# Optimization experiments

Measured on AMD Instinct MI355X. Metric: run time of the kernel, lower is better.

The kernel has to match this reference:

```python
import jax, jax.numpy as jnp
import numpy as np

B, T, H = 32, 4096, 512


def setup_inputs() -> dict:
    key = jax.random.key(0)
    k1, k2, k3, k4, k5 = jax.random.split(key, 5)
    stdv = 1.0 / np.sqrt(2 * H)
    stdv_v = 1.0 / np.sqrt(H)
    return {
        "hidden": jax.random.normal(k1, (B, H), dtype=jnp.float32),
        "encoder_outputs": jax.random.normal(k2, (T, B, H), dtype=jnp.float32),
        "W_attn": jax.random.uniform(k3, (H, 2 * H), minval=-stdv, maxval=stdv, dtype=jnp.float32),
        "b_attn": jax.random.uniform(k4, (H,), minval=-stdv, maxval=stdv, dtype=jnp.float32),
        "v": jax.random.uniform(k5, (H,), minval=-stdv_v, maxval=stdv_v, dtype=jnp.float32),
    }


def reference(hidden, encoder_outputs, W_attn, b_attn, v):
    # hidden: [B, H]; encoder_outputs: [T, B, H]
    T_ = encoder_outputs.shape[0]
    h = jnp.broadcast_to(hidden[None, :, :], (T_,) + hidden.shape).transpose(1, 0, 2)  # [B,T,H]
    enc = encoder_outputs.transpose(1, 0, 2)  # [B,T,H]
    cat = jnp.concatenate([h, enc], axis=2)  # [B,T,2H]
    # Linear(2H -> H) then legacy F.softmax with implicit dim=0 for 3D input (batch axis)
    energy = jax.nn.softmax(jnp.einsum('btk,hk->bth', cat, W_attn) + b_attn, axis=0)  # [B,T,H]
    # bmm(v[B,1,H], energy^T[B,H,T]) -> [B,1,T] -> squeeze -> [B,T]
    scores = jnp.einsum('h,bth->bt', v, energy)
    return jax.nn.relu(scores)[:, None, :]  # [B,1,T]
```

## Files before the change

### kernel.cpp

```cpp
#include <hip/hip_runtime.h>
#include <hip/hip_bf16.h>

#define B_ 32
#define T_ 4096
#define H_ 512
#define TILE_T 4
#define M_TILE 128
#define BK 64
#define KSTEPS 8
#define NTHREADS 512

typedef __attribute__((ext_vector_type(8))) short short8;
typedef __attribute__((ext_vector_type(8))) __bf16 bf16x8;
typedef __attribute__((ext_vector_type(4))) float f32x4;

__device__ __forceinline__ short f2bf(float f) {
    unsigned u = __builtin_bit_cast(unsigned, f);
    u = (u + 0x7fffu + ((u >> 16) & 1u)) >> 16;
    return (short)u;
}

__global__ void prep_w2(const float* __restrict__ W, short* __restrict__ w2p) {
    int idx = blockIdx.x * 256 + threadIdx.x;
    int kp = idx & 63;
    int h  = (idx >> 6) & 511;
    int s  = idx >> 15;
    int k  = kp ^ ((h & 7) << 3);
    w2p[idx] = f2bf(W[h * (2 * H_) + H_ + s * BK + k]);
}

__global__ void prep_hid(const float* __restrict__ hidden,
                         const float* __restrict__ W,
                         const float* __restrict__ bias,
                         float* __restrict__ hidproj) {
    __shared__ float hrow[H_];
    int b = blockIdx.y;
    int h = blockIdx.x * 128 + threadIdx.x;
    for (int i = threadIdx.x; i < H_; i += 128) hrow[i] = hidden[b * H_ + i];
    __syncthreads();
    const float* wr = W + (size_t)h * (2 * H_);
    float acc = bias[h];
#pragma unroll 4
    for (int k = 0; k < H_; k += 4) {
        acc += hrow[k]     * wr[k];
        acc += hrow[k + 1] * wr[k + 1];
        acc += hrow[k + 2] * wr[k + 2];
        acc += hrow[k + 3] * wr[k + 3];
    }
    hidproj[b * H_ + h] = acc;
}

__global__ __launch_bounds__(NTHREADS, 2)
void attn_main(const float* __restrict__ enc,
               const float* __restrict__ hidproj,
               const short* __restrict__ w2p,
               const float* __restrict__ vvec,
               float* __restrict__ out)
{
    __shared__ __align__(16) short lds_a[M_TILE * BK];
    __shared__ __align__(16) short lds_w[H_ * BK];

    const int tid  = threadIdx.x;
    const int lane = tid & 63;
    const int wid  = tid >> 6;
    const int t0   = blockIdx.x * TILE_T;
    const int n0   = wid * 64;
    const int lo   = lane & 15;
    const int hi4  = lane >> 4;

    f32x4 acc[8][4];
#pragma unroll
    for (int i = 0; i < 8; ++i)
#pragma unroll
        for (int j = 0; j < 4; ++j) acc[i][j] = f32x4{0.f, 0.f, 0.f, 0.f};

    const int s0row = tid >> 3;
    const int s0ks  = tid & 7;
    const float* encbase = enc + (size_t)(t0 * B_) * H_;

    for (int kk = 0; kk < KSTEPS; ++kk) {
        const short* wsrc = w2p + (size_t)kk * (H_ * BK);
#pragma unroll
        for (int r = 0; r < 8; ++r) {
            __builtin_amdgcn_global_load_lds(
                (const __attribute__((address_space(1))) void*)(wsrc + (r * 512 + tid) * 8),
                (__attribute__((address_space(3))) void*)(lds_w + (r * 512 + wid * 64) * 8),
                16, 0, 0);
        }
#pragma unroll
        for (int si = 0; si < 2; ++si) {
            int row = s0row + si * 64;
            const float* src = encbase + (size_t)row * H_ + kk * BK + s0ks * 8;
            f32x4 x0 = *(const f32x4*)(src);
            f32x4 x1 = *(const f32x4*)(src + 4);
            short8 pk;
            pk[0] = f2bf(x0[0]); pk[1] = f2bf(x0[1]); pk[2] = f2bf(x0[2]); pk[3] = f2bf(x0[3]);
            pk[4] = f2bf(x1[0]); pk[5] = f2bf(x1[1]); pk[6] = f2bf(x1[2]); pk[7] = f2bf(x1[3]);
            int kp = (s0ks ^ (row & 7)) * 8;
            *(short8*)&lds_a[row * BK + kp] = pk;
        }
        __syncthreads();

#pragma unroll
        for (int ks = 0; ks < 2; ++ks) {
            bf16x8 bfrag[4];
            int kbase = ks * 32 + hi4 * 8;
#pragma unroll
            for (int ni = 0; ni < 4; ++ni) {
                int hrow = n0 + ni * 16 + lo;
                int kp = kbase ^ ((hrow & 7) << 3);
                bfrag[ni] = *(const bf16x8*)&lds_w[hrow * BK + kp];
            }
#pragma unroll
            for (int mi = 0; mi < 8; ++mi) {
                int arow = mi * 16 + lo;
                int kp = kbase ^ ((arow & 7) << 3);
                bf16x8 afrag = *(const bf16x8*)&lds_a[arow * BK + kp];
#pragma unroll
                for (int ni = 0; ni < 4; ++ni)
                    acc[mi][ni] = __builtin_amdgcn_mfma_f32_16x16x32_bf16(
                        afrag, bfrag[ni], acc[mi][ni], 0, 0, 0);
            }
        }
        __syncthreads();
    }

    {
        float hp[2][4][4];
#pragma unroll
        for (int par = 0; par < 2; ++par)
#pragma unroll
            for (int j = 0; j < 4; ++j) {
                int b = par * 16 + hi4 * 4 + j;
#pragma unroll
                for (int ni = 0; ni < 4; ++ni)
                    hp[par][j][ni] = hidproj[b * H_ + n0 + ni * 16 + lo];
            }
#pragma unroll
        for (int mi = 0; mi < 8; ++mi)
#pragma unroll
            for (int ni = 0; ni < 4; ++ni)
#pragma unroll
                for (int j = 0; j < 4; ++j)
                    acc[mi][ni][j] += hp[mi & 1][j][ni];
    }

    float vh[4];
#pragma unroll
    for (int ni = 0; ni < 4; ++ni) vh[ni] = vvec[n0 + ni * 16 + lo];

    float scp[8][4];
#pragma unroll
    for (int tl = 0; tl < 4; ++tl) {
        const int m0 = tl * 2, m1 = tl * 2 + 1;
#pragma unroll
        for (int ni = 0; ni < 4; ++ni) {
            float mx = -1e30f;
#pragma unroll
            for (int j = 0; j < 4; ++j) {
                mx = fmaxf(mx, acc[m0][ni][j]);
                mx = fmaxf(mx, acc[m1][ni][j]);
            }
            mx = fmaxf(mx, __shfl_xor(mx, 16));
            mx = fmaxf(mx, __shfl_xor(mx, 32));
            float e0[4], e1[4];
            float sum = 0.f;
#pragma unroll
            for (int j = 0; j < 4; ++j) {
                e0[j] = __expf(acc[m0][ni][j] - mx);
                e1[j] = __expf(acc[m1][ni][j] - mx);
                sum += e0[j] + e1[j];
            }
            sum += __shfl_xor(sum, 16);
            sum += __shfl_xor(sum, 32);
            float rs = vh[ni] / sum;
#pragma unroll
            for (int j = 0; j < 4; ++j) {
                if (ni == 0) { scp[m0][j] = e0[j] * rs; scp[m1][j] = e1[j] * rs; }
                else         { scp[m0][j] += e0[j] * rs; scp[m1][j] += e1[j] * rs; }
            }
        }
    }

#pragma unroll
    for (int mi = 0; mi < 8; ++mi)
#pragma unroll
        for (int j = 0; j < 4; ++j) {
            float x = scp[mi][j];
            x += __shfl_xor(x, 1);
            x += __shfl_xor(x, 2);
            x += __shfl_xor(x, 4);
            x += __shfl_xor(x, 8);
            scp[mi][j] = x;
        }

    float* red = (float*)lds_a;
    if (lo == 0) {
#pragma unroll
        for (int mi = 0; mi < 8; ++mi)
#pragma unroll
            for (int j = 0; j < 4; ++j)
                red[wid * 128 + mi * 16 + hi4 * 4 + j] = scp[mi][j];
    }
    __syncthreads();
    if (tid < 128) {
        float s = 0.f;
#pragma unroll
        for (int w = 0; w < 8; ++w) s += red[w * 128 + tid];
        int b  = tid & 31;
        int tl = tid >> 5;
        out[(size_t)b * T_ + (t0 + tl)] = fmaxf(s, 0.f);
    }
}

extern "C" void kernel_launch(void* const* d_in, const int* in_sizes, int n_in,
                              void* d_out, int out_size, void* d_ws, size_t ws_size,
                              hipStream_t stream) {
    const float* hidden = (const float*)d_in[0];
    const float* enc    = (const float*)d_in[1];
    const float* W      = (const float*)d_in[2];
    const float* bias   = (const float*)d_in[3];
    const float* v      = (const float*)d_in[4];
    float* out = (float*)d_out;

    float* hidproj = (float*)d_ws;
    short* w2p     = (short*)((char*)d_ws + 65536);

    prep_w2<<<1024, 256, 0, stream>>>(W, w2p);
    prep_hid<<<dim3(4, 32), 128, 0, stream>>>(hidden, W, bias, hidproj);
    attn_main<<<T_ / TILE_T, NTHREADS, 0, stream>>>(enc, hidproj, w2p, v, out);
}
```

Measured before the change: 144.4 us.

## Double-buffer LDS tiles with BK=32 and prefetch next K-step during MFMA

Halves the K-step width to 32 and double-buffers both the weight and activation tiles in LDS. The next step's weight loads (global_load_lds) and encoder loads are issued before the current MFMAs, and one barrier per step replaces two. The activation tile now uses row padding (APAD=40) and the weight tile a 2-bit XOR swizzle to avoid bank conflicts. LDS use per block stays the same (about 74 KB), but twice as many K iterations and manual waitcnt tuning raise the risk of wrong waits.

```diff
diff --git a/kernel.cpp b/kernel.cpp
--- a/kernel.cpp
+++ b/kernel.cpp
@@ -6,8 +6,9 @@
 #define H_ 512
 #define TILE_T 4
 #define M_TILE 128
-#define BK 64
-#define KSTEPS 8
+#define BK 32
+#define KSTEPS 16
+#define APAD 40
 #define NTHREADS 512
 
 typedef __attribute__((ext_vector_type(8))) short short8;
@@ -22,10 +23,10 @@
 
 __global__ void prep_w2(const float* __restrict__ W, short* __restrict__ w2p) {
     int idx = blockIdx.x * 256 + threadIdx.x;
-    int kp = idx & 63;
-    int h  = (idx >> 6) & 511;
-    int s  = idx >> 15;
-    int k  = kp ^ ((h & 7) << 3);
+    int kp = idx & 31;
+    int h  = (idx >> 5) & 511;
+    int s  = idx >> 14;
+    int k  = ((kp >> 3) ^ ((h >> 1) & 3)) * 8 + (kp & 7);
     w2p[idx] = f2bf(W[h * (2 * H_) + H_ + s * BK + k]);
 }
 
@@ -57,8 +58,8 @@
                const float* __restrict__ vvec,
                float* __restrict__ out)
 {
-    __shared__ __align__(16) short lds_a[M_TILE * BK];
-    __shared__ __align__(16) short lds_w[H_ * BK];
+    __shared__ __align__(16) short lds_w[2][H_ * BK];
+    __shared__ __align__(16) short lds_a[2][M_TILE * APAD];
 
     const int tid  = threadIdx.x;
     const int lane = tid & 63;
@@ -67,6 +68,8 @@
     const int n0   = wid * 64;
     const int lo   = lane & 15;
     const int hi4  = lane >> 4;
+    const int wsw  = (lo >> 1) & 3;
+    const int wchunk = (hi4 ^ wsw) * 8;
 
     f32x4 acc[8][4];
 #pragma unroll
@@ -74,55 +77,74 @@
 #pragma unroll
         for (int j = 0; j < 4; ++j) acc[i][j] = f32x4{0.f, 0.f, 0.f, 0.f};
 
-    const int s0row = tid >> 3;
-    const int s0ks  = tid & 7;
-    const float* encbase = enc + (size_t)(t0 * B_) * H_;
-
-    for (int kk = 0; kk < KSTEPS; ++kk) {
-        const short* wsrc = w2p + (size_t)kk * (H_ * BK);
-#pragma unroll
-        for (int r = 0; r < 8; ++r) {
+    const int arow = tid >> 2;
+    const int akc  = tid & 3;
+    const float* asrc_base = enc + (size_t)(t0 * B_ + arow) * H_ + akc * 8;
+
+    {
+        const short* wsrc = w2p;
+#pragma unroll
+        for (int r = 0; r < 4; ++r) {
             __builtin_amdgcn_global_load_lds(
                 (const __attribute__((address_space(1))) void*)(wsrc + (r * 512 + tid) * 8),
-                (__attribute__((address_space(3))) void*)(lds_w + (r * 512 + wid * 64) * 8),
+                (__attribute__((address_space(3))) void*)(&lds_w[0][(r * 512 + wid * 64) * 8]),
                 16, 0, 0);
         }
-#pragma unroll
-        for (int si = 0; si < 2; ++si) {
-            int row = s0row + si * 64;
-            const float* src = encbase + (size_t)row * H_ + kk * BK + s0ks * 8;
-            f32x4 x0 = *(const f32x4*)(src);
-            f32x4 x1 = *(const f32x4*)(src + 4);
+        f32x4 x0 = *(const f32x4*)(asrc_base);
+        f32x4 x1 = *(const f32x4*)(asrc_base + 4);
+        short8 pk;
+        pk[0] = f2bf(x0[0]); pk[1] = f2bf(x0[1]); pk[2] = f2bf(x0[2]); pk[3] = f2bf(x0[3]);
+        pk[4] = f2bf(x1[0]); pk[5] = f2bf(x1[1]); pk[6] = f2bf(x1[2]); pk[7] = f2bf(x1[3]);
+        *(short8*)&lds_a[0][arow * APAD + akc * 8] = pk;
+    }
+
+    for (int kk = 0; kk < KSTEPS; ++kk) {
+        const int cur = kk & 1;
+        asm volatile("s_waitcnt lgkmcnt(0)" ::: "memory");
+        __builtin_amdgcn_s_barrier();
+
+        f32x4 x0, x1;
+        if (kk < KSTEPS - 1) {
+            const short* wsrc = w2p + (size_t)(kk + 1) * (H_ * BK);
+            short* wdst = &lds_w[cur ^ 1][0];
+#pragma unroll
+            for (int r = 0; r < 4; ++r) {
+                __builtin_amdgcn_global_load_lds(
+                    (const __attribute__((address_space(1))) void*)(wsrc + (r * 512 + tid) * 8),
+                    (__attribute__((address_space(3))) void*)(wdst + (r * 512 + wid * 64) * 8),
+                    16, 0, 0);
+            }
+            const float* asrc = asrc_base + (kk + 1) * BK;
+            x0 = *(const f32x4*)(asrc);
+            x1 = *(const f32x4*)(asrc + 4);
+            asm volatile("s_waitcnt vmcnt(6)" ::: "memory");
+        } else {
+            asm volatile("s_waitcnt vmcnt(0)" ::: "memory");
+        }
+
+        const short* __restrict__ wb = &lds_w[cur][0];
+        const short* __restrict__ ab = &lds_a[cur][0];
+        bf16x8 bfrag[4];
+#pragma unroll
+        for (int ni = 0; ni < 4; ++ni) {
+            int hrow = n0 + ni * 16 + lo;
+            bfrag[ni] = *(const bf16x8*)&wb[hrow * BK + wchunk];
+        }
+#pragma unroll
+        for (int mi = 0; mi < 8; ++mi) {
+            bf16x8 afrag = *(const bf16x8*)&ab[(mi * 16 + lo) * APAD + hi4 * 8];
+#pragma unroll
+            for (int ni = 0; ni < 4; ++ni)
+                acc[mi][ni] = __builtin_amdgcn_mfma_f32_16x16x32_bf16(
+                    afrag, bfrag[ni], acc[mi][ni], 0, 0, 0);
+        }
+
+        if (kk < KSTEPS - 1) {
             short8 pk;
             pk[0] = f2bf(x0[0]); pk[1] = f2bf(x0[1]); pk[2] = f2bf(x0[2]); pk[3] = f2bf(x0[3]);
             pk[4] = f2bf(x1[0]); pk[5] = f2bf(x1[1]); pk[6] = f2bf(x1[2]); pk[7] = f2bf(x1[3]);
-            int kp = (s0ks ^ (row & 7)) * 8;
-            *(short8*)&lds_a[row * BK + kp] = pk;
-        }
-        __syncthreads();
-
-#pragma unroll
-        for (int ks = 0; ks < 2; ++ks) {
-            bf16x8 bfrag[4];
-            int kbase = ks * 32 + hi4 * 8;
-#pragma unroll
-            for (int ni = 0; ni < 4; ++ni) {
-                int hrow = n0 + ni * 16 + lo;
-                int kp = kbase ^ ((hrow & 7) << 3);
-                bfrag[ni] = *(const bf16x8*)&lds_w[hrow * BK + kp];
-            }
-#pragma unroll
-            for (int mi = 0; mi < 8; ++mi) {
-                int arow = mi * 16 + lo;
-                int kp = kbase ^ ((arow & 7) << 3);
-                bf16x8 afrag = *(const bf16x8*)&lds_a[arow * BK + kp];
-#pragma unroll
-                for (int ni = 0; ni < 4; ++ni)
-                    acc[mi][ni] = __builtin_amdgcn_mfma_f32_16x16x32_bf16(
-                        afrag, bfrag[ni], acc[mi][ni], 0, 0, 0);
-            }
-        }
-        __syncthreads();
+            *(short8*)&lds_a[cur ^ 1][arow * APAD + akc * 8] = pk;
+        }
     }
 
     {
@@ -194,7 +216,8 @@
             scp[mi][j] = x;
         }
 
-    float* red = (float*)lds_a;
+    __syncthreads();
+    float* red = (float*)&lds_a[0][0];
     if (lo == 0) {
 #pragma unroll
         for (int mi = 0; mi < 8; ++mi)
```

Result: slower. 148.0 us (+2.5%).

## Double-buffer LDS tiles and interleave prefetch with MFMA phases

Applied to the files above, without the earlier changes.

Adds double-buffered LDS for the W and encoder tiles so the next K-step's global loads, covering both async global_load_lds for W and the fp32-to-bf16 conversion for A, are issued while the current step's MFMAs run. The K loop is split into four MFMA phases with explicit barriers, sched_barriers and setprio so loads and math interleave. It also changes the A-tile load mapping so each thread loads 16 contiguous floats. The aim is to hide global memory latency, at the cost of doubling LDS use (about 160KB), which may drop occupancy from 2 blocks/CU to 1.

```diff
diff --git a/kernel.cpp b/kernel.cpp
--- a/kernel.cpp
+++ b/kernel.cpp
@@ -25,8 +25,8 @@
     int kp = idx & 63;
     int h  = (idx >> 6) & 511;
     int s  = idx >> 15;
-    int k  = kp ^ ((h & 7) << 3);
-    w2p[idx] = f2bf(W[h * (2 * H_) + H_ + s * BK + k]);
+    int k  = s * BK + (((kp >> 3) ^ (h & 7)) << 3) + (kp & 7);
+    w2p[idx] = f2bf(W[h * (2 * H_) + H_ + k]);
 }
 
 __global__ void prep_hid(const float* __restrict__ hidden,
@@ -57,8 +57,8 @@
                const float* __restrict__ vvec,
                float* __restrict__ out)
 {
-    __shared__ __align__(16) short lds_a[M_TILE * BK];
-    __shared__ __align__(16) short lds_w[H_ * BK];
+    __shared__ __align__(16) short lds_w[2][H_ * BK];
+    __shared__ __align__(16) short lds_a[2][M_TILE * BK];
 
     const int tid  = threadIdx.x;
     const int lane = tid & 63;
@@ -74,56 +74,152 @@
 #pragma unroll
         for (int j = 0; j < 4; ++j) acc[i][j] = f32x4{0.f, 0.f, 0.f, 0.f};
 
-    const int s0row = tid >> 3;
-    const int s0ks  = tid & 7;
-    const float* encbase = enc + (size_t)(t0 * B_) * H_;
-
-    for (int kk = 0; kk < KSTEPS; ++kk) {
-        const short* wsrc = w2p + (size_t)kk * (H_ * BK);
+    const int arow = tid >> 2;
+    const int akc  = tid & 3;
+    const float* abase = enc + (size_t)(t0 * B_ + arow) * H_ + akc * 16;
+
+    {
+        const float* s = abase;
+        f32x4 x0 = *(const f32x4*)(s);
+        f32x4 x1 = *(const f32x4*)(s + 4);
+        f32x4 x2 = *(const f32x4*)(s + 8);
+        f32x4 x3 = *(const f32x4*)(s + 12);
 #pragma unroll
         for (int r = 0; r < 8; ++r) {
             __builtin_amdgcn_global_load_lds(
-                (const __attribute__((address_space(1))) void*)(wsrc + (r * 512 + tid) * 8),
-                (__attribute__((address_space(3))) void*)(lds_w + (r * 512 + wid * 64) * 8),
+                (const __attribute__((address_space(1))) void*)(w2p + r * 4096 + tid * 8),
+                (__attribute__((address_space(3))) void*)(&lds_w[0][r * 4096 + wid * 512]),
                 16, 0, 0);
         }
-#pragma unroll
-        for (int si = 0; si < 2; ++si) {
-            int row = s0row + si * 64;
-            const float* src = encbase + (size_t)row * H_ + kk * BK + s0ks * 8;
-            f32x4 x0 = *(const f32x4*)(src);
-            f32x4 x1 = *(const f32x4*)(src + 4);
-            short8 pk;
-            pk[0] = f2bf(x0[0]); pk[1] = f2bf(x0[1]); pk[2] = f2bf(x0[2]); pk[3] = f2bf(x0[3]);
-            pk[4] = f2bf(x1[0]); pk[5] = f2bf(x1[1]); pk[6] = f2bf(x1[2]); pk[7] = f2bf(x1[3]);
-            int kp = (s0ks ^ (row & 7)) * 8;
-            *(short8*)&lds_a[row * BK + kp] = pk;
-        }
+        short8 p0, p1;
+        p0[0]=f2bf(x0[0]); p0[1]=f2bf(x0[1]); p0[2]=f2bf(x0[2]); p0[3]=f2bf(x0[3]);
+        p0[4]=f2bf(x1[0]); p0[5]=f2bf(x1[1]); p0[6]=f2bf(x1[2]); p0[7]=f2bf(x1[3]);
+        p1[0]=f2bf(x2[0]); p1[1]=f2bf(x2[1]); p1[2]=f2bf(x2[2]); p1[3]=f2bf(x2[3]);
+        p1[4]=f2bf(x3[0]); p1[5]=f2bf(x3[1]); p1[6]=f2bf(x3[2]); p1[7]=f2bf(x3[3]);
+        *(short8*)&lds_a[0][arow * BK + (((2 * akc)     ^ (arow & 7)) << 3)] = p0;
+        *(short8*)&lds_a[0][arow * BK + (((2 * akc + 1) ^ (arow & 7)) << 3)] = p1;
         __syncthreads();
-
-#pragma unroll
-        for (int ks = 0; ks < 2; ++ks) {
-            bf16x8 bfrag[4];
-            int kbase = ks * 32 + hi4 * 8;
-#pragma unroll
-            for (int ni = 0; ni < 4; ++ni) {
-                int hrow = n0 + ni * 16 + lo;
-                int kp = kbase ^ ((hrow & 7) << 3);
-                bfrag[ni] = *(const bf16x8*)&lds_w[hrow * BK + kp];
-            }
-#pragma unroll
-            for (int mi = 0; mi < 8; ++mi) {
-                int arow = mi * 16 + lo;
-                int kp = kbase ^ ((arow & 7) << 3);
-                bf16x8 afrag = *(const bf16x8*)&lds_a[arow * BK + kp];
-#pragma unroll
-                for (int ni = 0; ni < 4; ++ni)
-                    acc[mi][ni] = __builtin_amdgcn_mfma_f32_16x16x32_bf16(
-                        afrag, bfrag[ni], acc[mi][ni], 0, 0, 0);
-            }
-        }
-        __syncthreads();
-    }
+    }
+
+#define PHASE_MFMA(AF, BF, MIBASE)                                              \
+    __builtin_amdgcn_s_barrier();                                               \
+    asm volatile("s_waitcnt lgkmcnt(0)" ::: "memory");                          \
+    __builtin_amdgcn_sched_barrier(0);                                          \
+    __builtin_amdgcn_s_setprio(1);                                              \
+    _Pragma("unroll")                                                           \
+    for (int mi = 0; mi < 4; ++mi)                                              \
+        _Pragma("unroll")                                                       \
+        for (int ni = 0; ni < 4; ++ni)                                          \
+            acc[(MIBASE) + mi][ni] = __builtin_amdgcn_mfma_f32_16x16x32_bf16(   \
+                AF[mi], BF[ni], acc[(MIBASE) + mi][ni], 0, 0, 0);               \
+    __builtin_amdgcn_s_setprio(0);                                              \
+    __builtin_amdgcn_sched_barrier(0);
+
+    for (int kk = 0; kk < KSTEPS; ++kk) {
+        const int cur = kk & 1;
+        const int nx  = kk + 1;
+        const bool pf = nx < KSTEPS;
+        const short* __restrict__ wb = &lds_w[cur][0];
+        const short* __restrict__ ab = &lds_a[cur][0];
+        short* __restrict__ wdst = &lds_w[cur ^ 1][0];
+        short* __restrict__ adst = &lds_a[cur ^ 1][0];
+        const short* wsrc = w2p + (size_t)nx * (H_ * BK);
+        const float* asrc = abase + (size_t)nx * BK;
+
+        f32x4 x0, x1, x2, x3;
+        bf16x8 b0[4], b1[4], af[4];
+
+#pragma unroll
+        for (int ni = 0; ni < 4; ++ni) {
+            int r = n0 + ni * 16 + lo;
+            b0[ni] = *(const bf16x8*)&wb[r * BK + (((hi4) ^ (r & 7)) << 3)];
+        }
+#pragma unroll
+        for (int mi = 0; mi < 4; ++mi) {
+            int r = mi * 16 + lo;
+            af[mi] = *(const bf16x8*)&ab[r * BK + (((hi4) ^ (r & 7)) << 3)];
+        }
+        if (pf) {
+            x0 = *(const f32x4*)(asrc);
+            x1 = *(const f32x4*)(asrc + 4);
+#pragma unroll
+            for (int r = 0; r < 2; ++r)
+                __builtin_amdgcn_global_load_lds(
+                    (const __attribute__((address_space(1))) void*)(wsrc + r * 4096 + tid * 8),
+                    (__attribute__((address_space(3))) void*)(wdst + r * 4096 + wid * 512),
+                    16, 0, 0);
+        }
+        PHASE_MFMA(af, b0, 0)
+        __builtin_amdgcn_s_barrier();
+
+#pragma unroll
+        for (int mi = 0; mi < 4; ++mi) {
+            int r = (mi + 4) * 16 + lo;
+            af[mi] = *(const bf16x8*)&ab[r * BK + (((hi4) ^ (r & 7)) << 3)];
+        }
+        if (pf) {
+            x2 = *(const f32x4*)(asrc + 8);
+            x3 = *(const f32x4*)(asrc + 12);
+#pragma unroll
+            for (int r = 2; r < 4; ++r)
+                __builtin_amdgcn_global_load_lds(
+                    (const __attribute__((address_space(1))) void*)(wsrc + r * 4096 + tid * 8),
+                    (__attribute__((address_space(3))) void*)(wdst + r * 4096 + wid * 512),
+                    16, 0, 0);
+        }
+        PHASE_MFMA(af, b0, 4)
+        __builtin_amdgcn_s_barrier();
+
+#pragma unroll
+        for (int ni = 0; ni < 4; ++ni) {
+            int r = n0 + ni * 16 + lo;
+            b1[ni] = *(const bf16x8*)&wb[r * BK + (((4 | hi4) ^ (r & 7)) << 3)];
+        }
+#pragma unroll
+        for (int mi = 0; mi < 4; ++mi) {
+            int r = mi * 16 + lo;
+            af[mi] = *(const bf16x8*)&ab[r * BK + (((4 | hi4) ^ (r & 7)) << 3)];
+        }
+        if (pf) {
+#pragma unroll
+            for (int r = 4; r < 6; ++r)
+                __builtin_amdgcn_global_load_lds(
+                    (const __attribute__((address_space(1))) void*)(wsrc + r * 4096 + tid * 8),
+                    (__attribute__((address_space(3))) void*)(wdst + r * 4096 + wid * 512),
+                    16, 0, 0);
+            short8 p0;
+            p0[0]=f2bf(x0[0]); p0[1]=f2bf(x0[1]); p0[2]=f2bf(x0[2]); p0[3]=f2bf(x0[3]);
+            p0[4]=f2bf(x1[0]); p0[5]=f2bf(x1[1]); p0[6]=f2bf(x1[2]); p0[7]=f2bf(x1[3]);
+            *(short8*)&adst[arow * BK + (((2 * akc) ^ (arow & 7)) << 3)] = p0;
+        }
+        PHASE_MFMA(af, b1, 0)
+        __builtin_amdgcn_s_barrier();
+
+#pragma unroll
+        for (int mi = 0; mi < 4; ++mi) {
+            int r = (mi + 4) * 16 + lo;
+            af[mi] = *(const bf16x8*)&ab[r * BK + (((4 | hi4) ^ (r & 7)) << 3)];
+        }
+        if (pf) {
+#pragma unroll
+            for (int r = 6; r < 8; ++r)
+                __builtin_amdgcn_global_load_lds(
+                    (const __attribute__((address_space(1))) void*)(wsrc + r * 4096 + tid * 8),
+                    (__attribute__((address_space(3))) void*)(wdst + r * 4096 + wid * 512),
+                    16, 0, 0);
+            short8 p1;
+            p1[0]=f2bf(x2[0]); p1[1]=f2bf(x2[1]); p1[2]=f2bf(x2[2]); p1[3]=f2bf(x2[3]);
+            p1[4]=f2bf(x3[0]); p1[5]=f2bf(x3[1]); p1[6]=f2bf(x3[2]); p1[7]=f2bf(x3[3]);
+            *(short8*)&adst[arow * BK + (((2 * akc + 1) ^ (arow & 7)) << 3)] = p1;
+        }
+        PHASE_MFMA(af, b1, 4)
+        if (pf) {
+            asm volatile("s_waitcnt vmcnt(0)" ::: "memory");
+            __builtin_amdgcn_sched_barrier(0);
+        }
+        __builtin_amdgcn_s_barrier();
+    }
+#undef PHASE_MFMA
 
     {
         float hp[2][4][4];
@@ -194,7 +290,8 @@
             scp[mi][j] = x;
         }
 
-    float* red = (float*)lds_a;
+    __syncthreads();
+    float* red = (float*)&lds_a[0][0];
     if (lo == 0) {
 #pragma unroll
         for (int mi = 0; mi < 8; ++mi)
```

Measured after the change: 140.8 us. 2.5% less time.

## Restructure main kernel into persistent double-buffered pipeline with register-fed W fragments

Applied to the files above, without the earlier changes.

The main kernel now launches 512 blocks. Each block handles four 64-row tiles (two time steps each) and stages the full K=512 encoder slab in double-buffered LDS, loading the next tile's fp32 activations during the current MFMA loop. W is pre-packed into MFMA fragment order so each wave reads its B fragments straight from global into registers with a 3-deep rotation, and the W staging through LDS is gone. A block-index swizzle, a new XOR layout and s_setprio around the MFMAs are also added. The aim is to remove the per-K-step barriers and W LDS traffic, at the cost of heavy register use (16 prefetch vectors plus fragments) and 128KB of LDS per block, which likely permits only one block per CU.

```diff
diff --git a/kernel.cpp b/kernel.cpp
--- a/kernel.cpp
+++ b/kernel.cpp
@@ -4,13 +4,12 @@
 #define B_ 32
 #define T_ 4096
 #define H_ 512
-#define TILE_T 4
-#define M_TILE 128
-#define BK 64
-#define KSTEPS 8
+#define MT 64
+#define TPB 4
+#define NBLK 512
 #define NTHREADS 512
 
-typedef __attribute__((ext_vector_type(8))) short short8;
+typedef __attribute__((ext_vector_type(4))) short short4v;
 typedef __attribute__((ext_vector_type(8))) __bf16 bf16x8;
 typedef __attribute__((ext_vector_type(4))) float f32x4;
 
@@ -20,13 +19,16 @@
     return (short)u;
 }
 
-__global__ void prep_w2(const float* __restrict__ W, short* __restrict__ w2p) {
+__global__ void prep_w2f(const float* __restrict__ W, short* __restrict__ w2f) {
     int idx = blockIdx.x * 256 + threadIdx.x;
-    int kp = idx & 63;
-    int h  = (idx >> 6) & 511;
-    int s  = idx >> 15;
-    int k  = kp ^ ((h & 7) << 3);
-    w2p[idx] = f2bf(W[h * (2 * H_) + H_ + s * BK + k]);
+    int j    = idx & 7;
+    int lane = (idx >> 3) & 63;
+    int ni   = (idx >> 9) & 3;
+    int ck   = (idx >> 11) & 15;
+    int c    = (idx >> 15) & 7;
+    int h = c * 64 + ni * 16 + (lane & 15);
+    int k = ck * 32 + (lane >> 4) * 8 + j;
+    w2f[idx] = f2bf(W[h * (2 * H_) + H_ + k]);
 }
 
 __global__ void prep_hid(const float* __restrict__ hidden,
@@ -53,163 +55,199 @@
 __global__ __launch_bounds__(NTHREADS, 2)
 void attn_main(const float* __restrict__ enc,
                const float* __restrict__ hidproj,
-               const short* __restrict__ w2p,
+               const short* __restrict__ w2f,
                const float* __restrict__ vvec,
                float* __restrict__ out)
 {
-    __shared__ __align__(16) short lds_a[M_TILE * BK];
-    __shared__ __align__(16) short lds_w[H_ * BK];
+    __shared__ __align__(16) short lds_a[2][MT * H_];
+    __shared__ float red[2][NTHREADS];
 
     const int tid  = threadIdx.x;
     const int lane = tid & 63;
     const int wid  = tid >> 6;
-    const int t0   = blockIdx.x * TILE_T;
-    const int n0   = wid * 64;
     const int lo   = lane & 15;
     const int hi4  = lane >> 4;
 
-    f32x4 acc[8][4];
-#pragma unroll
-    for (int i = 0; i < 8; ++i)
-#pragma unroll
-        for (int j = 0; j < 4; ++j) acc[i][j] = f32x4{0.f, 0.f, 0.f, 0.f};
-
-    const int s0row = tid >> 3;
-    const int s0ks  = tid & 7;
-    const float* encbase = enc + (size_t)(t0 * B_) * H_;
-
-    for (int kk = 0; kk < KSTEPS; ++kk) {
-        const short* wsrc = w2p + (size_t)kk * (H_ * BK);
-#pragma unroll
-        for (int r = 0; r < 8; ++r) {
-            __builtin_amdgcn_global_load_lds(
-                (const __attribute__((address_space(1))) void*)(wsrc + (r * 512 + tid) * 8),
-                (__attribute__((address_space(3))) void*)(lds_w + (r * 512 + wid * 64) * 8),
-                16, 0, 0);
-        }
-#pragma unroll
-        for (int si = 0; si < 2; ++si) {
-            int row = s0row + si * 64;
-            const float* src = encbase + (size_t)row * H_ + kk * BK + s0ks * 8;
-            f32x4 x0 = *(const f32x4*)(src);
-            f32x4 x1 = *(const f32x4*)(src + 4);
-            short8 pk;
-            pk[0] = f2bf(x0[0]); pk[1] = f2bf(x0[1]); pk[2] = f2bf(x0[2]); pk[3] = f2bf(x0[3]);
-            pk[4] = f2bf(x1[0]); pk[5] = f2bf(x1[1]); pk[6] = f2bf(x1[2]); pk[7] = f2bf(x1[3]);
-            int kp = (s0ks ^ (row & 7)) * 8;
-            *(short8*)&lds_a[row * BK + kp] = pk;
-        }
-        __syncthreads();
-
-#pragma unroll
-        for (int ks = 0; ks < 2; ++ks) {
-            bf16x8 bfrag[4];
-            int kbase = ks * 32 + hi4 * 8;
-#pragma unroll
-            for (int ni = 0; ni < 4; ++ni) {
-                int hrow = n0 + ni * 16 + lo;
-                int kp = kbase ^ ((hrow & 7) << 3);
-                bfrag[ni] = *(const bf16x8*)&lds_w[hrow * BK + kp];
-            }
-#pragma unroll
-            for (int mi = 0; mi < 8; ++mi) {
-                int arow = mi * 16 + lo;
-                int kp = kbase ^ ((arow & 7) << 3);
-                bf16x8 afrag = *(const bf16x8*)&lds_a[arow * BK + kp];
+    const int bid  = blockIdx.x;
+    const int bswz = (bid & 7) * (NBLK / 8) + (bid >> 3);
+    const int gbase = bswz * TPB;
+
+    const short* wbase = w2f + (size_t)wid * 32768 + lane * 8;
+
+    const int th  = tid >> 7;
+    const int gq  = (tid & 127) >> 1;
+    const int sub = (tid & 1) * 8;
+    const int gb2 = gq ^ ((gq >> 3) & 7) ^ th;
+    const int wconst = th * 1024 + sub;
+    const int aoff   = th * H_ + (tid & 127) * 4;
+
+    float vh[4];
+#pragma unroll
+    for (int ni = 0; ni < 4; ++ni) vh[ni] = vvec[wid * 64 + ni * 16 + lo];
+
+    {
+        const float* ap = enc + (size_t)gbase * (MT * H_) + aoff;
+        f32x4 xs[16];
+#pragma unroll
+        for (int j = 0; j < 16; ++j) xs[j] = *(const f32x4*)(ap + j * 2048);
+#pragma unroll
+        for (int j = 0; j < 16; ++j) {
+            short4v p;
+            p[0] = f2bf(xs[j][0]); p[1] = f2bf(xs[j][1]);
+            p[2] = f2bf(xs[j][2]); p[3] = f2bf(xs[j][3]);
+            int gp = gb2 ^ ((j & 1) << 2);
+            *(short4v*)((char*)&lds_a[0][0] + j * 4096 + wconst + gp * 16) = p;
+        }
+        asm volatile("s_waitcnt lgkmcnt(0)" ::: "memory");
+        __builtin_amdgcn_s_barrier();
+    }
+
+    for (int lt = 0; lt < TPB; ++lt) {
+        const int g   = gbase + lt;
+        const int buf = lt & 1;
+        const short* __restrict__ ab = &lds_a[buf][0];
+        short* __restrict__ adst = &lds_a[buf ^ 1][0];
+        const bool pf = (lt + 1) < TPB;
+
+        f32x4 acc[4][4];
+#pragma unroll
+        for (int i = 0; i < 4; ++i)
+#pragma unroll
+            for (int j = 0; j < 4; ++j) acc[i][j] = f32x4{0.f, 0.f, 0.f, 0.f};
+
+        bf16x8 bq[3][4];
+#pragma unroll
+        for (int ni = 0; ni < 4; ++ni) bq[0][ni] = *(const bf16x8*)(wbase + (0 * 4 + ni) * 512);
+#pragma unroll
+        for (int ni = 0; ni < 4; ++ni) bq[1][ni] = *(const bf16x8*)(wbase + (1 * 4 + ni) * 512);
+
+        f32x4 xs[16];
+        const float* ap = enc + (size_t)(g + 1) * (MT * H_) + aoff;
+
+#pragma unroll
+        for (int c = 0; c < 16; ++c) {
+            if (c == 0 && pf) {
+#pragma unroll
+                for (int j = 0; j < 16; ++j) xs[j] = *(const f32x4*)(ap + j * 2048);
+            }
+            if (c + 2 < 16) {
+#pragma unroll
+                for (int ni = 0; ni < 4; ++ni)
+                    bq[(c + 2) % 3][ni] = *(const bf16x8*)(wbase + ((c + 2) * 4 + ni) * 512);
+            }
+            bf16x8 af[4];
+#pragma unroll
+            for (int mi = 0; mi < 4; ++mi) {
+                int row = mi * 16 + lo;
+                int gg  = c * 4 + hi4;
+                int gp  = gg ^ ((gg >> 3) & 7) ^ (lo & 7);
+                af[mi] = *(const bf16x8*)&ab[row * H_ + gp * 8];
+            }
+            __builtin_amdgcn_s_setprio(1);
+#pragma unroll
+            for (int mi = 0; mi < 4; ++mi)
 #pragma unroll
                 for (int ni = 0; ni < 4; ++ni)
                     acc[mi][ni] = __builtin_amdgcn_mfma_f32_16x16x32_bf16(
-                        afrag, bfrag[ni], acc[mi][ni], 0, 0, 0);
-            }
-        }
-        __syncthreads();
-    }
-
-    {
-        float hp[2][4][4];
-#pragma unroll
-        for (int par = 0; par < 2; ++par)
+                        af[mi], bq[c % 3][ni], acc[mi][ni], 0, 0, 0);
+            __builtin_amdgcn_s_setprio(0);
+            if (pf && c >= 8 && (c & 1) == 0) {
+                const int j0 = ((c - 8) >> 1) << 2;
+#pragma unroll
+                for (int jj = 0; jj < 4; ++jj) {
+                    const int j = j0 + jj;
+                    short4v p;
+                    p[0] = f2bf(xs[j][0]); p[1] = f2bf(xs[j][1]);
+                    p[2] = f2bf(xs[j][2]); p[3] = f2bf(xs[j][3]);
+                    int gp = gb2 ^ ((j & 1) << 2);
+                    *(short4v*)((char*)adst + j * 4096 + wconst + gp * 16) = p;
+                }
+            }
+        }
+
+        {
+            float hp[2][4][4];
+#pragma unroll
+            for (int par = 0; par < 2; ++par)
+#pragma unroll
+                for (int j = 0; j < 4; ++j) {
+                    int b = par * 16 + hi4 * 4 + j;
+#pragma unroll
+                    for (int ni = 0; ni < 4; ++ni)
+                        hp[par][j][ni] = hidproj[b * H_ + wid * 64 + ni * 16 + lo];
+                }
+#pragma unroll
+            for (int mi = 0; mi < 4; ++mi)
+#pragma unroll
+                for (int ni = 0; ni < 4; ++ni)
+#pragma unroll
+                    for (int j = 0; j < 4; ++j)
+                        acc[mi][ni][j] += hp[mi & 1][j][ni];
+        }
+
+        float scp[4][4];
+#pragma unroll
+        for (int tl2 = 0; tl2 < 2; ++tl2) {
+            const int m0 = tl2 * 2, m1 = tl2 * 2 + 1;
+#pragma unroll
+            for (int ni = 0; ni < 4; ++ni) {
+                float mx = -1e30f;
+#pragma unroll
+                for (int j = 0; j < 4; ++j) {
+                    mx = fmaxf(mx, acc[m0][ni][j]);
+                    mx = fmaxf(mx, acc[m1][ni][j]);
+                }
+                mx = fmaxf(mx, __shfl_xor(mx, 16));
+                mx = fmaxf(mx, __shfl_xor(mx, 32));
+                float e0[4], e1[4];
+                float sum = 0.f;
+#pragma unroll
+                for (int j = 0; j < 4; ++j) {
+                    e0[j] = __expf(acc[m0][ni][j] - mx);
+                    e1[j] = __expf(acc[m1][ni][j] - mx);
+                    sum += e0[j] + e1[j];
+                }
+                sum += __shfl_xor(sum, 16);
+                sum += __shfl_xor(sum, 32);
+                float rs = vh[ni] / sum;
+#pragma unroll
+                for (int j = 0; j < 4; ++j) {
+                    if (ni == 0) { scp[m0][j] = e0[j] * rs; scp[m1][j] = e1[j] * rs; }
+                    else         { scp[m0][j] += e0[j] * rs; scp[m1][j] += e1[j] * rs; }
+                }
+            }
+        }
+
+#pragma unroll
+        for (int mi = 0; mi < 4; ++mi)
 #pragma unroll
             for (int j = 0; j < 4; ++j) {
-                int b = par * 16 + hi4 * 4 + j;
-#pragma unroll
-                for (int ni = 0; ni < 4; ++ni)
-                    hp[par][j][ni] = hidproj[b * H_ + n0 + ni * 16 + lo];
-            }
-#pragma unroll
-        for (int mi = 0; mi < 8; ++mi)
-#pragma unroll
-            for (int ni = 0; ni < 4; ++ni)
+                float x = scp[mi][j];
+                x += __shfl_xor(x, 1);
+                x += __shfl_xor(x, 2);
+                x += __shfl_xor(x, 4);
+                x += __shfl_xor(x, 8);
+                scp[mi][j] = x;
+            }
+
+        if (lo == 0) {
+#pragma unroll
+            for (int mi = 0; mi < 4; ++mi)
 #pragma unroll
                 for (int j = 0; j < 4; ++j)
-                    acc[mi][ni][j] += hp[mi & 1][j][ni];
-    }
-
-    float vh[4];
-#pragma unroll
-    for (int ni = 0; ni < 4; ++ni) vh[ni] = vvec[n0 + ni * 16 + lo];
-
-    float scp[8][4];
-#pragma unroll
-    for (int tl = 0; tl < 4; ++tl) {
-        const int m0 = tl * 2, m1 = tl * 2 + 1;
-#pragma unroll
-        for (int ni = 0; ni < 4; ++ni) {
-            float mx = -1e30f;
-#pragma unroll
-            for (int j = 0; j < 4; ++j) {
-                mx = fmaxf(mx, acc[m0][ni][j]);
-                mx = fmaxf(mx, acc[m1][ni][j]);
-            }
-            mx = fmaxf(mx, __shfl_xor(mx, 16));
-            mx = fmaxf(mx, __shfl_xor(mx, 32));
-            float e0[4], e1[4];
-            float sum = 0.f;
-#pragma unroll
-            for (int j = 0; j < 4; ++j) {
-                e0[j] = __expf(acc[m0][ni][j] - mx);
-                e1[j] = __expf(acc[m1][ni][j] - mx);
-                sum += e0[j] + e1[j];
-            }
-            sum += __shfl_xor(sum, 16);
-            sum += __shfl_xor(sum, 32);
-            float rs = vh[ni] / sum;
-#pragma unroll
-            for (int j = 0; j < 4; ++j) {
-                if (ni == 0) { scp[m0][j] = e0[j] * rs; scp[m1][j] = e1[j] * rs; }
-                else         { scp[m0][j] += e0[j] * rs; scp[m1][j] += e1[j] * rs; }
-            }
-        }
-    }
-
-#pragma unroll
-    for (int mi = 0; mi < 8; ++mi)
-#pragma unroll
-        for (int j = 0; j < 4; ++j) {
-            float x = scp[mi][j];
-            x += __shfl_xor(x, 1);
-            x += __shfl_xor(x, 2);
-            x += __shfl_xor(x, 4);
-            x += __shfl_xor(x, 8);
-            scp[mi][j] = x;
-        }
-
-    float* red = (float*)lds_a;
-    if (lo == 0) {
-#pragma unroll
-        for (int mi = 0; mi < 8; ++mi)
-#pragma unroll
-            for (int j = 0; j < 4; ++j)
-                red[wid * 128 + mi * 16 + hi4 * 4 + j] = scp[mi][j];
-    }
-    __syncthreads();
-    if (tid < 128) {
-        float s = 0.f;
-#pragma unroll
-        for (int w = 0; w < 8; ++w) s += red[w * 128 + tid];
-        int b  = tid & 31;
-        int tl = tid >> 5;
-        out[(size_t)b * T_ + (t0 + tl)] = fmaxf(s, 0.f);
+                    red[buf][wid * 64 + mi * 16 + hi4 * 4 + j] = scp[mi][j];
+        }
+        asm volatile("s_waitcnt lgkmcnt(0)" ::: "memory");
+        __builtin_amdgcn_s_barrier();
+
+        if (tid < MT) {
+            float s = 0.f;
+#pragma unroll
+            for (int w = 0; w < 8; ++w) s += red[buf][w * 64 + tid];
+            int b   = tid & 31;
+            int tl2 = tid >> 5;
+            out[(size_t)b * T_ + (g * 2 + tl2)] = fmaxf(s, 0.f);
+        }
     }
 }
 
@@ -224,9 +262,9 @@
     float* out = (float*)d_out;
 
     float* hidproj = (float*)d_ws;
-    short* w2p     = (short*)((char*)d_ws + 65536);
-
-    prep_w2<<<1024, 256, 0, stream>>>(W, w2p);
+    short* w2f     = (short*)((char*)d_ws + 65536);
+
+    prep_w2f<<<1024, 256, 0, stream>>>(W, w2f);
     prep_hid<<<dim3(4, 32), 128, 0, stream>>>(hidden, W, bias, hidproj);
-    attn_main<<<T_ / TILE_T, NTHREADS, 0, stream>>>(enc, hidproj, w2p, v, out);
-}
+    attn_main<<<NBLK, NTHREADS, 0, stream>>>(enc, hidproj, w2f, v, out);
+}
```

After: 300.1 us. 108% more time.
